# Optimization experiments

Hardware: AMD Instinct MI355X
Metric: run time of the kernel (lower is better)

Reference implementation:

```python
import jax, jax.numpy as jnp
import numpy as np

B, S, D, H = 1, 2048, 4096, 32
HD = D // H
THETA = 10000.0
IN_SCALE = 0.1   # input_scale buffer
Q_SCALE = 0.1    # q_proj_scale buffer
K_SCALE = 0.1    # k_proj_scale buffer
V_SCALE = 0.1    # v_proj_scale buffer
OUT_SCALE = 0.1  # out_input_scale buffer


def _fake_q(x, scale, lo, hi):
    # round-to-int + clamp, kept in float (faithful to int8 fake-quant)
    return jnp.clip(jnp.round(x / scale), lo, hi)


def _w4a8_linear(x, qw, w_scale, in_scale):
    # int8 fake-quantized activation x int4-valued weight, dequant output
    qx = _fake_q(x, in_scale, -128, 127)
    return jnp.einsum('bsd,od->bso', qx, qw) * (in_scale * w_scale)


def _rope_tables(position_ids):
    inv_freq = 1.0 / (THETA ** (jnp.arange(0, HD, 2, dtype=jnp.float32) / HD))
    ang = position_ids.astype(jnp.float32)[..., None] * inv_freq  # [B,S,HD/2]
    emb = jnp.concatenate([ang, ang], axis=-1)                     # [B,S,HD]
    return jnp.cos(emb)[:, None], jnp.sin(emb)[:, None]            # [B,1,S,HD]


def _rotate_half(x):
    return jnp.concatenate([-x[..., HD // 2:], x[..., :HD // 2]], axis=-1)


def setup_inputs() -> dict:
    key = jax.random.key(0)
    ks = jax.random.split(key, 9)
    hidden_states = jax.random.normal(ks[0], (B, S, D), jnp.float32)
    def int4_w(k):
        return jnp.round(jax.random.uniform(k, (D, D), jnp.float32, -8.0, 7.0))
    def ch_scale(k):
        return jax.random.uniform(k, (D,), jnp.float32, 0.01, 0.03)
    wq, wk, wv, wo = int4_w(ks[1]), int4_w(ks[2]), int4_w(ks[3]), int4_w(ks[4])
    sq_w, sk_w, sv_w, so_w = ch_scale(ks[5]), ch_scale(ks[6]), ch_scale(ks[7]), ch_scale(ks[8])
    position_ids = jnp.arange(S, dtype=jnp.int32)[None, :]
    causal = jnp.tril(jnp.ones((S, S), dtype=bool))
    attention_mask = jnp.where(causal, 0.0, -1e9).astype(jnp.float32)[None, None]
    return dict(hidden_states=hidden_states, wq=wq, wk=wk, wv=wv, wo=wo,
                sq_w=sq_w, sk_w=sk_w, sv_w=sv_w, so_w=so_w,
                attention_mask=attention_mask, position_ids=position_ids)


def reference(hidden_states, wq, wk, wv, wo, sq_w, sk_w, sv_w, so_w,
              attention_mask, position_ids):
    # W4A8 dequant projections
    q = _w4a8_linear(hidden_states, wq, sq_w, IN_SCALE)
    k = _w4a8_linear(hidden_states, wk, sk_w, IN_SCALE)
    v = _w4a8_linear(hidden_states, wv, sv_w, IN_SCALE)
    q = q.reshape(B, S, H, HD).transpose(0, 2, 1, 3)  # [B,H,S,HD]
    k = k.reshape(B, S, H, HD).transpose(0, 2, 1, 3)
    v = v.reshape(B, S, H, HD).transpose(0, 2, 1, 3)
    # RoPE
    cos, sin = _rope_tables(position_ids)
    q = q * cos + _rotate_half(q) * sin
    k = k * cos + _rotate_half(k) * sin
    # int8 fake-quant of q/k/v, then dequant before matmuls
    q = _fake_q(q, Q_SCALE, -128, 127)
    k = _fake_q(k, K_SCALE, -128, 127)
    v = _fake_q(v, V_SCALE, -128, 127)
    scores = jnp.einsum('bhqd,bhkd->bhqk', q * Q_SCALE, k * K_SCALE) / np.sqrt(HD)
    scores = scores + attention_mask
    attn = jax.nn.softmax(scores.astype(jnp.float32), axis=-1)
    out = jnp.einsum('bhqk,bhkd->bhqd', attn, v * V_SCALE)
    out = out.transpose(0, 2, 1, 3).reshape(B, S, D)
    # o_proj input re-quantized to int8 with out_input_scale (clamp -127..127)
    out_q = _fake_q(out, OUT_SCALE, -127, 127)
    attn_output = jnp.einsum('bsd,od->bso', out_q, wo) * (OUT_SCALE * so_w)
    return attn_output
```

## Files before the change

### kernel.cpp

```cpp
#include <hip/hip_runtime.h>
#include <math.h>
#include <stdint.h>

#define S_LEN 2048
#define D_DIM 4096
#define NHEAD 32
#define HDIM  128

typedef int      v4i __attribute__((ext_vector_type(4)));
typedef float    v4f __attribute__((ext_vector_type(4)));
typedef _Float16 v8h __attribute__((ext_vector_type(8)));

__device__ __forceinline__ float quant128(float x) {
  return fminf(fmaxf(rintf(x / 0.1f), -128.f), 127.f);
}
__device__ __forceinline__ void gl_lds16(const void* g, void* l) {
  __builtin_amdgcn_global_load_lds(
      (const __attribute__((address_space(1))) void*)g,
      (__attribute__((address_space(3))) void*)l, 16, 0, 0);
}

__global__ __launch_bounds__(256) void quant_hidden_k(const float* __restrict__ in,
                                                      int8_t* __restrict__ out) {
  const int idx = blockIdx.x * 256 + threadIdx.x;
  const float4 v = ((const float4*)in)[idx];
  const int q0 = (int)quant128(v.x), q1 = (int)quant128(v.y);
  const int q2 = (int)quant128(v.z), q3 = (int)quant128(v.w);
  ((int*)out)[idx] = (q0 & 0xff) | ((q1 & 0xff) << 8) | ((q2 & 0xff) << 16) | ((q3 & 0xff) << 24);
}

__global__ __launch_bounds__(256) void wconv3_k(const float* __restrict__ a,
                                                const float* __restrict__ b,
                                                const float* __restrict__ c,
                                                int8_t* __restrict__ out) {
  const int which = blockIdx.x >> 14;
  const int sub = blockIdx.x & 16383;
  const float* src = (which == 0) ? a : (which == 1) ? b : c;
  const int idx = sub * 256 + threadIdx.x;
  const float4 v = ((const float4*)src)[idx];
  const int q0 = __float2int_rn(v.x), q1 = __float2int_rn(v.y);
  const int q2 = __float2int_rn(v.z), q3 = __float2int_rn(v.w);
  ((int*)out)[(size_t)which * 4194304 + idx] =
      (q0 & 0xff) | ((q1 & 0xff) << 8) | ((q2 & 0xff) << 16) | ((q3 & 0xff) << 24);
}

__global__ __launch_bounds__(256) void wconv_k(const float* __restrict__ in,
                                               int8_t* __restrict__ out) {
  const int idx = blockIdx.x * 256 + threadIdx.x;
  const float4 v = ((const float4*)in)[idx];
  const int q0 = __float2int_rn(v.x), q1 = __float2int_rn(v.y);
  const int q2 = __float2int_rn(v.z), q3 = __float2int_rn(v.w);
  ((int*)out)[idx] = (q0 & 0xff) | ((q1 & 0xff) << 8) | ((q2 & 0xff) << 16) | ((q3 & 0xff) << 24);
}

__global__ __launch_bounds__(256) void rope_tab_k(const int* __restrict__ pos,
                                                  float* __restrict__ ct,
                                                  float* __restrict__ st) {
  const int idx = blockIdx.x * 256 + threadIdx.x;
  const int s = idx >> 6, j = idx & 63;
  const float inv = exp2f((float)j * -0.20762050593046016f);
  const float a = (float)pos[s] * inv;
  float si, c;
  sincosf(a, &si, &c);
  ct[idx] = c;
  st[idx] = si;
}

template <int MODE>
__device__ __forceinline__ void gemm_body(
    int8_t* __restrict__ LS, const int8_t* __restrict__ A8,
    const int8_t* __restrict__ W8, const float* __restrict__ s0,
    const float* __restrict__ s1, const float* __restrict__ s2,
    const float* __restrict__ ctab, const float* __restrict__ stab,
    void* __restrict__ out0, void* __restrict__ out1, void* __restrict__ out2,
    int nwg) {
  int8_t* const Abase = LS;
  int8_t* const Bbase = LS + 49152;

  const int t = threadIdx.x;
  const int w = t >> 6, lane = t & 63, g = lane >> 4, l15 = lane & 15;
  const int wm = w >> 2, wn = w & 3;

  const int bid = blockIdx.x;
  const int lb = (bid & 7) * (nwg >> 3) + (bid >> 3);
  const int within = lb & 15, g16 = lb >> 4;
  const int bm = ((g16 & 3) * 4 + (within >> 2)) * 128;
  const int bn = ((g16 >> 2) * 4 + (within & 3)) * 256;

  const int rowo = lane >> 3;
  const int schunk = ((lane & 7) ^ rowo) * 16;
  const int8_t* srcA[2];
  const int8_t* srcB[4];
#pragma unroll
  for (int i = 0; i < 2; ++i)
    srcA[i] = A8 + (size_t)(bm + w * 16 + i * 8 + rowo) * D_DIM + schunk;
#pragma unroll
  for (int i = 0; i < 4; ++i)
    srcB[i] = W8 + (size_t)(bn + w * 32 + i * 8 + rowo) * D_DIM + schunk;

#define STAGE(KT, BI)                                                       \
  {                                                                         \
    const int kof_ = (KT) * 128;                                            \
    int8_t* Ad_ = Abase + (BI) * 16384 + w * 2048;                          \
    int8_t* Bd_ = Bbase + (BI) * 32768 + w * 4096;                          \
    _Pragma("unroll") for (int i_ = 0; i_ < 2; ++i_)                        \
        gl_lds16(srcA[i_] + kof_, Ad_ + i_ * 1024);                         \
    _Pragma("unroll") for (int i_ = 0; i_ < 4; ++i_)                        \
        gl_lds16(srcB[i_] + kof_, Bd_ + i_ * 1024);                         \
  }

  const int nc0 = (wn & 1) * 32 + (wn >> 1) * 128;

  const int coff0 = (g ^ (l15 & 7)) * 16;
  const int coff1 = ((4 | g) ^ (l15 & 7)) * 16;
  const int aoff = (wm * 64 + l15) * 128;
  int boff[4];
#pragma unroll
  for (int ni = 0; ni < 4; ++ni)
    boff[ni] = (nc0 + (ni & 1) * 16 + (ni >> 1) * 64 + l15) * 128;

  v4i fa[4], fb[4];
  v4i ga[4], gb[4];

#define RD(FA, FB, BI, COFF)                                                \
  {                                                                         \
    const int8_t* Ab_ = Abase + (BI) * 16384;                               \
    const int8_t* Bb_ = Bbase + (BI) * 32768;                               \
    _Pragma("unroll") for (int mi_ = 0; mi_ < 4; ++mi_)                     \
        FA[mi_] = *(const v4i*)(Ab_ + aoff + mi_ * 2048 + (COFF));          \
    _Pragma("unroll") for (int ni_ = 0; ni_ < 4; ++ni_)                     \
        FB[ni_] = *(const v4i*)(Bb_ + boff[ni_] + (COFF));                  \
  }

#define MM(FA, FB)                                                          \
  _Pragma("unroll") for (int mi_ = 0; mi_ < 4; ++mi_)                       \
  _Pragma("unroll") for (int ni_ = 0; ni_ < 4; ++ni_)                       \
      acc[mi_][ni_] = __builtin_amdgcn_mfma_i32_16x16x64_i8(                \
          FA[mi_], FB[ni_], acc[mi_][ni_], 0, 0, 0);

  v4i acc[4][4];
#pragma unroll
  for (int mi = 0; mi < 4; ++mi)
#pragma unroll
    for (int ni = 0; ni < 4; ++ni) acc[mi][ni] = (v4i){0, 0, 0, 0};

  STAGE(0, 0)
  STAGE(1, 1)
  asm volatile("s_waitcnt vmcnt(6)" ::: "memory");
  __builtin_amdgcn_s_barrier();
  __builtin_amdgcn_sched_barrier(0);
  RD(fa, fb, 0, coff0)

  for (int t3 = 0; t3 < 33; t3 += 3) {
#pragma unroll
    for (int u = 0; u < 3; ++u) {
      const int kt = t3 + u;
      if (kt < 32) {
        if (kt + 2 < 32) STAGE(kt + 2, ((u + 2) % 3))
        RD(ga, gb, u, coff1)
        __builtin_amdgcn_s_setprio(1);
        MM(fa, fb)
        MM(ga, gb)
        __builtin_amdgcn_s_setprio(0);
        if (kt + 2 < 32)
          asm volatile("s_waitcnt vmcnt(6)" ::: "memory");
        else
          asm volatile("s_waitcnt vmcnt(0)" ::: "memory");
        __builtin_amdgcn_s_barrier();
        __builtin_amdgcn_sched_barrier(0);
        if (kt + 1 < 32) RD(fa, fb, ((u + 1) % 3), coff0)
      }
    }
  }
#undef STAGE
#undef RD
#undef MM

  const int srow0 = bm + wm * 64;
  if (MODE == 1) {
    float* dst = (float*)out0;
#pragma unroll
    for (int ni = 0; ni < 4; ++ni) {
      const int col = bn + nc0 + (ni & 1) * 16 + (ni >> 1) * 64 + l15;
      const float sc = 0.1f * s0[col];
#pragma unroll
      for (int mi = 0; mi < 4; ++mi)
#pragma unroll
        for (int r = 0; r < 4; ++r)
          dst[(size_t)(srow0 + mi * 16 + g * 4 + r) * D_DIM + col] =
              (float)acc[mi][ni][r] * sc;
    }
  } else {
    const int seg = bn >> 12;
    const int bcol = bn & 4095;
    if (seg == 2) {
      _Float16* dst = (_Float16*)out2;
#pragma unroll
      for (int ni = 0; ni < 4; ++ni) {
        const int col = bcol + nc0 + (ni & 1) * 16 + (ni >> 1) * 64 + l15;
        const float scv = 0.1f * s2[col];
#pragma unroll
        for (int mi = 0; mi < 4; ++mi)
#pragma unroll
          for (int r = 0; r < 4; ++r) {
            const int s = srow0 + mi * 16 + g * 4 + r;
            dst[(size_t)col * S_LEN + s] = (_Float16)quant128((float)acc[mi][ni][r] * scv);
          }
      }
    } else {
      const float* wsc = seg ? s1 : s0;
      int8_t* dst = seg ? (int8_t*)out1 : (int8_t*)out0;
      const int hb = bcol + (wn >> 1) * 128;
#pragma unroll
      for (int ni = 0; ni < 2; ++ni) {
        const int dlo = (wn & 1) * 32 + ni * 16 + l15;
        const int clo = hb + dlo;
        const float sc0 = 0.1f * wsc[clo];
        const float sc1 = 0.1f * wsc[clo + 64];
#pragma unroll
        for (int mi = 0; mi < 4; ++mi)
#pragma unroll
          for (int r = 0; r < 4; ++r) {
            const int s = srow0 + mi * 16 + g * 4 + r;
            const float c = ctab[s * 64 + dlo];
            const float si = stab[s * 64 + dlo];
            const float x1 = (float)acc[mi][ni][r] * sc0;
            const float x2 = (float)acc[mi][ni + 2][r] * sc1;
            dst[(size_t)s * D_DIM + clo] = (int8_t)quant128(x1 * c - x2 * si);
            dst[(size_t)s * D_DIM + clo + 64] = (int8_t)quant128(x2 * c + x1 * si);
          }
      }
    }
  }
}

__global__ __launch_bounds__(512) void gemm_qkv(
    const int8_t* __restrict__ A8, const int8_t* __restrict__ W8,
    const float* __restrict__ s0, const float* __restrict__ s1,
    const float* __restrict__ s2, const float* __restrict__ ctab,
    const float* __restrict__ stab, void* __restrict__ out0,
    void* __restrict__ out1, void* __restrict__ out2) {
  __shared__ __align__(16) int8_t LS[3 * 16384 + 3 * 32768];
  gemm_body<0>(LS, A8, W8, s0, s1, s2, ctab, stab, out0, out1, out2, 768);
}

__global__ __launch_bounds__(512) void gemm_out(
    const int8_t* __restrict__ A8, const int8_t* __restrict__ W8,
    const float* __restrict__ s0, const float* __restrict__ ctab,
    const float* __restrict__ stab, void* __restrict__ out0) {
  __shared__ __align__(16) int8_t LS[3 * 16384 + 3 * 32768];
  gemm_body<1>(LS, A8, W8, s0, s0, s0, ctab, stab, out0, out0, out0, 256);
}

__global__ __launch_bounds__(512, 4) void attn_v9(
    const int8_t* __restrict__ q8, const int8_t* __restrict__ k8,
    const _Float16* __restrict__ vT, int8_t* __restrict__ o8) {
  __shared__ __align__(16) int8_t Kls[3][8192];
  __shared__ __align__(16) int8_t Vls[3][16384];
  const int h = blockIdx.y;
  const int jj = (h < 16) ? (15 - blockIdx.x) : blockIdx.x;
  const int t = threadIdx.x;
  const int w = t >> 6, lane = t & 63, g = lane >> 4, l15 = lane & 15;
  const int T = 2 * jj + 2;
  const int q0 = (jj * 8 + w) * 16;
  const int q_lane = q0 + l15;
  const float SSCALE = 8.838834764831845e-4f;
  const v8h vones = {(_Float16)1, (_Float16)1, (_Float16)1, (_Float16)1,
                     (_Float16)1, (_Float16)1, (_Float16)1, (_Float16)1};

  const int ks_slot = t >> 3;
  const int ks_cs = (t & 7) ^ (ks_slot & 7);
  const int ks_key = ((ks_slot >> 5) & 1) * 32 + ((ks_slot >> 3) & 1) * 16 +
                     ((ks_slot >> 2) & 1) * 8 + ((ks_slot >> 4) & 1) * 4 +
                     (ks_slot & 3);
  const int k_src = ks_key * D_DIM + ks_cs * 16;
  const int k_dst = t * 16;
  int v_src[2], v_dst[2];
#pragma unroll
  for (int i = 0; i < 2; ++i) {
    const int lin = i * 512 + t;
    const int d = lin >> 3;
    const int cs = (lin & 7) ^ (d & 7);
    v_src[i] = d * S_LEN + cs * 8;
    v_dst[i] = lin * 16;
  }
  const int8_t* kbg = k8 + (size_t)h * HDIM;
  const _Float16* vbg = vT + (size_t)h * HDIM * S_LEN;

  auto stage = [&](int kt, int b) {
    const int8_t* ks = kbg + (size_t)kt * (64 * D_DIM);
    const _Float16* vs = vbg + kt * 64;
    gl_lds16(ks + k_src, &Kls[b][k_dst]);
#pragma unroll
    for (int i = 0; i < 2; ++i) gl_lds16(vs + v_src[i], &Vls[b][v_dst[i]]);
  };

  const v4i qa0 = *(const v4i*)(q8 + (size_t)q_lane * D_DIM + h * HDIM + g * 16);
  const v4i qa1 = *(const v4i*)(q8 + (size_t)q_lane * D_DIM + h * HDIM + 64 + g * 16);

  v4f o[8];
#pragma unroll
  for (int n = 0; n < 8; ++n) o[n] = (v4f){0.f, 0.f, 0.f, 0.f};
  v4f lacc = (v4f){0.f, 0.f, 0.f, 0.f};
  float m_i = -INFINITY;

  stage(0, 0);
  if (T > 1) stage(1, 1);

  int bi = 0;
  for (int kt = 0; kt < T; ++kt) {
    if (kt + 1 < T)
      asm volatile("s_waitcnt vmcnt(3)" ::: "memory");
    else
      asm volatile("s_waitcnt vmcnt(0)" ::: "memory");
    __builtin_amdgcn_s_barrier();
    __builtin_amdgcn_sched_barrier(0);
    if (kt + 2 < T) stage(kt + 2, bi >= 1 ? bi - 1 : bi + 2);

    const int ksw = (l15 & 7);
    float sc[4][4];
#pragma unroll
    for (int nt = 0; nt < 4; ++nt) {
      const int8_t* kr = &Kls[bi][(nt * 16 + l15) * 128];
      const v4i kb0 = *(const v4i*)(kr + ((g ^ ksw) * 16));
      const v4i kb1 = *(const v4i*)(kr + (((4 + g) ^ ksw) * 16));
      v4i c = (v4i){0, 0, 0, 0};
      c = __builtin_amdgcn_mfma_i32_16x16x64_i8(kb0, qa0, c, 0, 0, 0);
      c = __builtin_amdgcn_mfma_i32_16x16x64_i8(kb1, qa1, c, 0, 0, 0);
#pragma unroll
      for (int r = 0; r < 4; ++r) {
        float s = (float)c[r] * SSCALE;
        if (kt >= T - 2) {
          const int key = kt * 64 + ((nt >> 1) << 5) + ((g >> 1) << 4) +
                          ((g & 1) << 3) + ((nt & 1) << 2) + r;
          if (key > q_lane) s = -1.0e30f;
        }
        sc[nt][r] = s;
      }
    }
    float mx = fmaxf(fmaxf(fmaxf(sc[0][0], sc[0][1]), fmaxf(sc[0][2], sc[0][3])),
                     fmaxf(fmaxf(sc[1][0], sc[1][1]), fmaxf(sc[1][2], sc[1][3])));
    mx = fmaxf(mx, fmaxf(fmaxf(fmaxf(sc[2][0], sc[2][1]), fmaxf(sc[2][2], sc[2][3])),
                         fmaxf(fmaxf(sc[3][0], sc[3][1]), fmaxf(sc[3][2], sc[3][3]))));
    mx = fmaxf(mx, __shfl_xor(mx, 16));
    mx = fmaxf(mx, __shfl_xor(mx, 32));
    const float mnew = fmaxf(m_i, mx);
    const float alpha = __expf(m_i - mnew);
    m_i = mnew;

    float p[4][4];
#pragma unroll
    for (int nt = 0; nt < 4; ++nt)
#pragma unroll
      for (int r = 0; r < 4; ++r) p[nt][r] = __expf(sc[nt][r] - m_i);

    v8h ph0, ph1;
#pragma unroll
    for (int e = 0; e < 8; ++e) {
      ph0[e] = (_Float16)p[e >> 2][e & 3];
      ph1[e] = (_Float16)p[2 + (e >> 2)][e & 3];
    }
    float a_r[4];
#pragma unroll
    for (int r = 0; r < 4; ++r)
      a_r[r] = __shfl(alpha, (lane & 48) | (g * 4 + r));
#pragma unroll
    for (int n = 0; n < 8; ++n)
#pragma unroll
      for (int r = 0; r < 4; ++r) o[n][r] *= a_r[r];
#pragma unroll
    for (int r = 0; r < 4; ++r) lacc[r] *= a_r[r];

    __builtin_amdgcn_s_setprio(1);
    lacc = __builtin_amdgcn_mfma_f32_16x16x32_f16(ph0, vones, lacc, 0, 0, 0);
    lacc = __builtin_amdgcn_mfma_f32_16x16x32_f16(ph1, vones, lacc, 0, 0, 0);
#pragma unroll
    for (int nt = 0; nt < 8; ++nt) {
      const int8_t* vr = &Vls[bi][(nt * 16 + l15) * 128];
      const v8h v0 = *(const v8h*)(vr + ((g ^ ksw) * 16));
      const v8h v1 = *(const v8h*)(vr + (((4 + g) ^ ksw) * 16));
      o[nt] = __builtin_amdgcn_mfma_f32_16x16x32_f16(ph0, v0, o[nt], 0, 0, 0);
      o[nt] = __builtin_amdgcn_mfma_f32_16x16x32_f16(ph1, v1, o[nt], 0, 0, 0);
    }
    __builtin_amdgcn_s_setprio(0);

    bi = (bi == 2) ? 0 : bi + 1;
  }

#pragma unroll
  for (int r = 0; r < 4; ++r) {
    const float rL = 1.0f / lacc[r];
    const size_t row = (size_t)(q0 + g * 4 + r) * D_DIM + h * HDIM;
#pragma unroll
    for (int nt = 0; nt < 8; ++nt) {
      const int q = (int)fminf(fmaxf(rintf(o[nt][r] * rL), -127.f), 127.f);
      o8[row + nt * 16 + l15] = (int8_t)q;
    }
  }
}

extern "C" void kernel_launch(void* const* d_in, const int* in_sizes, int n_in,
                              void* d_out, int out_size, void* d_ws, size_t ws_size,
                              hipStream_t stream) {
  (void)in_sizes; (void)n_in; (void)out_size; (void)ws_size;
  const float* hidden = (const float*)d_in[0];
  const float* wq = (const float*)d_in[1];
  const float* wk = (const float*)d_in[2];
  const float* wv = (const float*)d_in[3];
  const float* wo = (const float*)d_in[4];
  const float* sq = (const float*)d_in[5];
  const float* sk = (const float*)d_in[6];
  const float* sv = (const float*)d_in[7];
  const float* so = (const float*)d_in[8];
  const int* pos = (const int*)d_in[10];
  float* out = (float*)d_out;

  char* ws = (char*)d_ws;
  int8_t* h8 = (int8_t*)ws;
  int8_t* q8 = (int8_t*)(ws + (8ull << 20));
  int8_t* k8 = (int8_t*)(ws + (16ull << 20));
  _Float16* vT = (_Float16*)(ws + (24ull << 20));
  int8_t* w8a = (int8_t*)(ws + (40ull << 20));
  int8_t* w8b = (int8_t*)(ws + (56ull << 20));
  int8_t* w8c = (int8_t*)(ws + (72ull << 20));
  float* ctab = (float*)(ws + (88ull << 20));
  float* stab = (float*)(ws + (88ull << 20) + (512ull << 10));
  int8_t* o8 = h8;

  hipLaunchKernelGGL(rope_tab_k, dim3(512), dim3(256), 0, stream, pos, ctab, stab);
  hipLaunchKernelGGL(quant_hidden_k, dim3(8192), dim3(256), 0, stream, hidden, h8);
  hipLaunchKernelGGL(wconv3_k, dim3(49152), dim3(256), 0, stream, wq, wk, wv, w8a);

  hipLaunchKernelGGL(gemm_qkv, dim3(768), dim3(512), 0, stream, h8, w8a,
                     sq, sk, sv, ctab, stab, (void*)q8, (void*)k8, (void*)vT);
  hipLaunchKernelGGL(wconv_k, dim3(16384), dim3(256), 0, stream, wo, w8a);
  hipLaunchKernelGGL(attn_v9, dim3(16, 32), dim3(512), 0, stream, q8, k8, vT, o8);
  hipLaunchKernelGGL(gemm_out, dim3(256), dim3(512), 0, stream, o8, w8a,
                     so, ctab, stab, (void*)out);
}
```

Baseline: 487.6 us.

## Store V as int8 and compute PV with int8 MFMA using quantized probabilities

The QKV GEMM now writes the transposed V as int8 instead of fp16. The attention kernel quantizes the softmax probabilities to int8 (scaled by 127) and runs both P·V and the row-sum denominator with i8 16x16x64 MFMAs. Each tile's integer result is rescaled and accumulated into float registers. This halves V global and LDS traffic and the number of PV MFMA instructions, and the K/V LDS layouts and swizzles are adjusted to match. In exchange, quantizing P to 127 levels adds numerical error, which could flip rounding in the final int8 requantization, and per-tile integer-to-float conversion work is added.

```diff
diff --git a/kernel.cpp b/kernel.cpp
--- a/kernel.cpp
+++ b/kernel.cpp
@@ -194,7 +194,7 @@
     const int seg = bn >> 12;
     const int bcol = bn & 4095;
     if (seg == 2) {
-      _Float16* dst = (_Float16*)out2;
+      int8_t* dst = (int8_t*)out2;
 #pragma unroll
       for (int ni = 0; ni < 4; ++ni) {
         const int col = bcol + nc0 + (ni & 1) * 16 + (ni >> 1) * 64 + l15;
@@ -204,7 +204,7 @@
 #pragma unroll
           for (int r = 0; r < 4; ++r) {
             const int s = srow0 + mi * 16 + g * 4 + r;
-            dst[(size_t)col * S_LEN + s] = (_Float16)quant128((float)acc[mi][ni][r] * scv);
+            dst[(size_t)col * S_LEN + s] = (int8_t)quant128((float)acc[mi][ni][r] * scv);
           }
       }
     } else {
@@ -252,11 +252,11 @@
   gemm_body<1>(LS, A8, W8, s0, s0, s0, ctab, stab, out0, out0, out0, 256);
 }
 
-__global__ __launch_bounds__(512, 4) void attn_v9(
+__global__ __launch_bounds__(512, 4) void attn_v10(
     const int8_t* __restrict__ q8, const int8_t* __restrict__ k8,
-    const _Float16* __restrict__ vT, int8_t* __restrict__ o8) {
+    const int8_t* __restrict__ vT, int8_t* __restrict__ o8) {
   __shared__ __align__(16) int8_t Kls[3][8192];
-  __shared__ __align__(16) int8_t Vls[3][16384];
+  __shared__ __align__(16) int8_t Vls[3][8192];
   const int h = blockIdx.y;
   const int jj = (h < 16) ? (15 - blockIdx.x) : blockIdx.x;
   const int t = threadIdx.x;
@@ -265,34 +265,24 @@
   const int q0 = (jj * 8 + w) * 16;
   const int q_lane = q0 + l15;
   const float SSCALE = 8.838834764831845e-4f;
-  const v8h vones = {(_Float16)1, (_Float16)1, (_Float16)1, (_Float16)1,
-                     (_Float16)1, (_Float16)1, (_Float16)1, (_Float16)1};
+  const v4i vones1 = {0x01010101, 0x01010101, 0x01010101, 0x01010101};
 
   const int ks_slot = t >> 3;
   const int ks_cs = (t & 7) ^ (ks_slot & 7);
-  const int ks_key = ((ks_slot >> 5) & 1) * 32 + ((ks_slot >> 3) & 1) * 16 +
-                     ((ks_slot >> 2) & 1) * 8 + ((ks_slot >> 4) & 1) * 4 +
+  const int ks_key = ((ks_slot >> 2) & 3) * 16 + ((ks_slot >> 4) & 3) * 4 +
                      (ks_slot & 3);
   const int k_src = ks_key * D_DIM + ks_cs * 16;
   const int k_dst = t * 16;
-  int v_src[2], v_dst[2];
-#pragma unroll
-  for (int i = 0; i < 2; ++i) {
-    const int lin = i * 512 + t;
-    const int d = lin >> 3;
-    const int cs = (lin & 7) ^ (d & 7);
-    v_src[i] = d * S_LEN + cs * 8;
-    v_dst[i] = lin * 16;
-  }
+  const int vrow = t >> 2;
+  const int v_src = vrow * S_LEN + ((t & 3) ^ ((vrow >> 1) & 3)) * 16;
+  const int v_dst = t * 16;
+
   const int8_t* kbg = k8 + (size_t)h * HDIM;
-  const _Float16* vbg = vT + (size_t)h * HDIM * S_LEN;
+  const int8_t* vbg = vT + (size_t)h * HDIM * S_LEN;
 
   auto stage = [&](int kt, int b) {
-    const int8_t* ks = kbg + (size_t)kt * (64 * D_DIM);
-    const _Float16* vs = vbg + kt * 64;
-    gl_lds16(ks + k_src, &Kls[b][k_dst]);
-#pragma unroll
-    for (int i = 0; i < 2; ++i) gl_lds16(vs + v_src[i], &Vls[b][v_dst[i]]);
+    gl_lds16(kbg + (size_t)kt * (64 * D_DIM) + k_src, &Kls[b][k_dst]);
+    gl_lds16(vbg + kt * 64 + v_src, &Vls[b][v_dst]);
   };
 
   const v4i qa0 = *(const v4i*)(q8 + (size_t)q_lane * D_DIM + h * HDIM + g * 16);
@@ -310,7 +300,7 @@
   int bi = 0;
   for (int kt = 0; kt < T; ++kt) {
     if (kt + 1 < T)
-      asm volatile("s_waitcnt vmcnt(3)" ::: "memory");
+      asm volatile("s_waitcnt vmcnt(2)" ::: "memory");
     else
       asm volatile("s_waitcnt vmcnt(0)" ::: "memory");
     __builtin_amdgcn_s_barrier();
@@ -331,8 +321,7 @@
       for (int r = 0; r < 4; ++r) {
         float s = (float)c[r] * SSCALE;
         if (kt >= T - 2) {
-          const int key = kt * 64 + ((nt >> 1) << 5) + ((g >> 1) << 4) +
-                          ((g & 1) << 3) + ((nt & 1) << 2) + r;
+          const int key = kt * 64 + g * 16 + nt * 4 + r;
           if (key > q_lane) s = -1.0e30f;
         }
         sc[nt][r] = s;
@@ -354,33 +343,33 @@
 #pragma unroll
       for (int r = 0; r < 4; ++r) p[nt][r] = __expf(sc[nt][r] - m_i);
 
-    v8h ph0, ph1;
-#pragma unroll
-    for (int e = 0; e < 8; ++e) {
-      ph0[e] = (_Float16)p[e >> 2][e & 3];
-      ph1[e] = (_Float16)p[2 + (e >> 2)][e & 3];
+    v4i pa;
+#pragma unroll
+    for (int nt = 0; nt < 4; ++nt) {
+      int d = 0;
+#pragma unroll
+      for (int r = 0; r < 4; ++r)
+        d |= (__float2int_rn(p[nt][r] * 127.f) & 0xff) << (8 * r);
+      pa[nt] = d;
     }
     float a_r[4];
 #pragma unroll
     for (int r = 0; r < 4; ++r)
       a_r[r] = __shfl(alpha, (lane & 48) | (g * 4 + r));
-#pragma unroll
-    for (int n = 0; n < 8; ++n)
-#pragma unroll
-      for (int r = 0; r < 4; ++r) o[n][r] *= a_r[r];
-#pragma unroll
-    for (int r = 0; r < 4; ++r) lacc[r] *= a_r[r];
-
+
+    const int vco = (g ^ ((l15 >> 1) & 3)) * 16;
     __builtin_amdgcn_s_setprio(1);
-    lacc = __builtin_amdgcn_mfma_f32_16x16x32_f16(ph0, vones, lacc, 0, 0, 0);
-    lacc = __builtin_amdgcn_mfma_f32_16x16x32_f16(ph1, vones, lacc, 0, 0, 0);
+    const v4i lden =
+        __builtin_amdgcn_mfma_i32_16x16x64_i8(pa, vones1, (v4i){0, 0, 0, 0}, 0, 0, 0);
+#pragma unroll
+    for (int r = 0; r < 4; ++r) lacc[r] = lacc[r] * a_r[r] + (float)lden[r];
 #pragma unroll
     for (int nt = 0; nt < 8; ++nt) {
-      const int8_t* vr = &Vls[bi][(nt * 16 + l15) * 128];
-      const v8h v0 = *(const v8h*)(vr + ((g ^ ksw) * 16));
-      const v8h v1 = *(const v8h*)(vr + (((4 + g) ^ ksw) * 16));
-      o[nt] = __builtin_amdgcn_mfma_f32_16x16x32_f16(ph0, v0, o[nt], 0, 0, 0);
-      o[nt] = __builtin_amdgcn_mfma_f32_16x16x32_f16(ph1, v1, o[nt], 0, 0, 0);
+      const v4i vb = *(const v4i*)(&Vls[bi][(nt * 16 + l15) * 64] + vco);
+      const v4i pv =
+          __builtin_amdgcn_mfma_i32_16x16x64_i8(pa, vb, (v4i){0, 0, 0, 0}, 0, 0, 0);
+#pragma unroll
+      for (int r = 0; r < 4; ++r) o[nt][r] = o[nt][r] * a_r[r] + (float)pv[r];
     }
     __builtin_amdgcn_s_setprio(0);
 
@@ -419,7 +408,7 @@
   int8_t* h8 = (int8_t*)ws;
   int8_t* q8 = (int8_t*)(ws + (8ull << 20));
   int8_t* k8 = (int8_t*)(ws + (16ull << 20));
-  _Float16* vT = (_Float16*)(ws + (24ull << 20));
+  int8_t* vT = (int8_t*)(ws + (24ull << 20));
   int8_t* w8a = (int8_t*)(ws + (40ull << 20));
   int8_t* w8b = (int8_t*)(ws + (56ull << 20));
   int8_t* w8c = (int8_t*)(ws + (72ull << 20));
@@ -434,7 +423,7 @@
   hipLaunchKernelGGL(gemm_qkv, dim3(768), dim3(512), 0, stream, h8, w8a,
                      sq, sk, sv, ctab, stab, (void*)q8, (void*)k8, (void*)vT);
   hipLaunchKernelGGL(wconv_k, dim3(16384), dim3(256), 0, stream, wo, w8a);
-  hipLaunchKernelGGL(attn_v9, dim3(16, 32), dim3(512), 0, stream, q8, k8, vT, o8);
+  hipLaunchKernelGGL(attn_v10, dim3(16, 32), dim3(512), 0, stream, q8, k8, vT, o8);
   hipLaunchKernelGGL(gemm_out, dim3(256), dim3(512), 0, stream, o8, w8a,
                      so, ctab, stab, (void*)out);
 }
```

Result: no change. 492.2 us (+0.9%).
